# Performance work log

Measured on AMD Instinct MI355X. Metric: run time of the kernel, lower is better.

The kernel has to match this reference:

```python
import jax, jax.numpy as jnp
import numpy as np

N_HEAD = 16
T_THRESHOLD = 0.001


def setup_inputs() -> dict:
    key = jax.random.key(0)
    k_x, k_wa, k_ba, k_wp, k_bp = jax.random.split(key, 5)
    B, P, L, R = 8, 1024, 4, 256
    C = L * R  # n_embd = 1024
    s = 1.0 / np.sqrt(C)
    return {
        "x": jax.random.normal(k_x, (B, P, L, R), dtype=jnp.float32),
        "w_attn": jax.random.normal(k_wa, (C, 3 * C), dtype=jnp.float32) * s,
        "b_attn": jax.random.normal(k_ba, (3 * C,), dtype=jnp.float32) * 0.01,
        "w_proj": jax.random.normal(k_wp, (C, C), dtype=jnp.float32) * s,
        "b_proj": jax.random.normal(k_bp, (C,), dtype=jnp.float32) * 0.01,
    }


def reference(x, w_attn, b_attn, w_proj, b_proj):
    B, P, L, R = x.shape
    C = L * R
    H = N_HEAD
    hd = C // H
    xf = x.reshape(B, P, C)                      # (B, T, C)
    qkv = xf @ w_attn + b_attn                   # (B, T, 3C)
    q, k, v = jnp.split(qkv, 3, axis=-1)
    # (B, H, T, hd)
    q = q.reshape(B, P, H, hd).transpose(0, 2, 1, 3)
    k = k.reshape(B, P, H, hd).transpose(0, 2, 1, 3)
    v = v.reshape(B, P, H, hd).transpose(0, 2, 1, 3)
    att = jnp.einsum("bhqd,bhkd->bhqk", q, k) * (1.0 / np.sqrt(hd))
    att = jax.nn.softmax(att, axis=-1)
    att = jax.nn.relu(att - T_THRESHOLD)         # post-softmax thresholding
    y = jnp.einsum("bhqk,bhkd->bhqd", att, v)    # (B, H, T, hd)
    y = y.transpose(0, 2, 1, 3).reshape(B, P, C)
    y = y @ w_proj + b_proj
    return y.reshape(B, P, L, R)
```

## Files before the change

kernel.cpp:

```cpp
#include <hip/hip_runtime.h>


typedef _Float16 half8 __attribute__((ext_vector_type(8)));
typedef _Float16 half4_t __attribute__((ext_vector_type(4)));
typedef float floatx4 __attribute__((ext_vector_type(4)));
typedef float floatx16 __attribute__((ext_vector_type(16)));
typedef unsigned int uint4v __attribute__((ext_vector_type(4)));

__device__ __forceinline__ void gl2lds16(const void* gsrc, void* lds) {
    __builtin_amdgcn_global_load_lds(
        (const __attribute__((address_space(1))) unsigned int*)gsrc,
        (__attribute__((address_space(3))) unsigned int*)lds,
        16, 0, 0);
}

__device__ __forceinline__ unsigned pkh(float a, float b) {
    _Float16 ha = (_Float16)a, hb = (_Float16)b;
    unsigned short ua = __builtin_bit_cast(unsigned short, ha);
    unsigned short ub = __builtin_bit_cast(unsigned short, hb);
    return (unsigned)ua | ((unsigned)ub << 16);
}

__global__ __launch_bounds__(256) void prep(const float4* __restrict__ x4,
                                            _Float16* __restrict__ xh,
                                            const float* __restrict__ wa,
                                            _Float16* __restrict__ waT,
                                            const float* __restrict__ wp,
                                            _Float16* __restrict__ wpT) {
    __shared__ _Float16 t[64 * 65];
    int bid = blockIdx.x;
    if (bid < 4096) {
        int idx = bid * 256 + threadIdx.x;
#pragma unroll
        for (int i = idx; i < 2097152; i += 1048576) {
            float4 v = x4[i];
            half4_t h = { (_Float16)v.x, (_Float16)v.y, (_Float16)v.z, (_Float16)v.w };
            *(half4_t*)(xh + (size_t)i * 4) = h;
        }
    } else {
        int tt = bid - 4096;
        int by = tt & 15, bx = tt >> 4;
        const float* in = wa; _Float16* out = waT; int C = 3072;
        if (bx >= 48) { bx -= 48; in = wp; out = wpT; C = 1024; }
#pragma unroll
        for (int it = 0; it < 16; ++it) {
            int idx = it * 256 + threadIdx.x;
            int r = idx >> 6, c = idx & 63;
            t[c * 65 + r] = (_Float16)in[(size_t)(by * 64 + r) * C + bx * 64 + c];
        }
        __syncthreads();
#pragma unroll
        for (int it = 0; it < 16; ++it) {
            int idx = it * 256 + threadIdx.x;
            int rn = idx >> 6, ck = idx & 63;
            out[(size_t)(bx * 64 + rn) * 1024 + by * 64 + ck] = t[rn * 65 + ck];
        }
    }
}

#define GBAR __builtin_amdgcn_s_barrier()
#define WLGKM do { asm volatile("s_waitcnt lgkmcnt(0)" ::: "memory"); } while (0)
#define WVM2  do { asm volatile("s_waitcnt vmcnt(2)"   ::: "memory"); } while (0)
#define WVM4  do { asm volatile("s_waitcnt vmcnt(4)"   ::: "memory"); } while (0)
#define WVM0  do { asm volatile("s_waitcnt vmcnt(0)"   ::: "memory"); } while (0)


#define WLDA(buf, rg)                                                                         \
    do {                                                                                      \
        _Pragma("unroll") for (int i = 0; i < 4; ++i) {                                       \
            int r_ = wm * 128 + ((rg) * 4 + i) * 16 + l15;                                    \
            _Pragma("unroll") for (int kk = 0; kk < 2; ++kk)                                  \
                a[i][kk] = *(const half8*)(sA + (buf) * 32768 + r_ * 128 +                    \
                                           ((((kk << 2) + quad) ^ (r_ & 7)) << 4));           \
        }                                                                                     \
    } while (0)

#define WLDB(buf, cg, bb)                                                                     \
    do {                                                                                      \
        _Pragma("unroll") for (int j = 0; j < 2; ++j) {                                       \
            int r_ = wn * 64 + ((cg) * 2 + j) * 16 + l15;                                     \
            _Pragma("unroll") for (int kk = 0; kk < 2; ++kk)                                  \
                bb[j][kk] = *(const half8*)(sB + (buf) * 32768 + r_ * 128 +                   \
                                            ((((kk << 2) + quad) ^ (r_ & 7)) << 4));          \
        }                                                                                     \
    } while (0)

#define WMMA(rg, cg, bb)                                                                      \
    do {                                                                                      \
        __builtin_amdgcn_s_setprio(1);                                                        \
        _Pragma("unroll") for (int kk = 0; kk < 2; ++kk)                                      \
            _Pragma("unroll") for (int i = 0; i < 4; ++i)                                     \
                _Pragma("unroll") for (int j = 0; j < 2; ++j)                                  \
                    acc[(rg) * 4 + i][(cg) * 2 + j] = __builtin_amdgcn_mfma_f32_16x16x32_f16( \
                        a[i][kk], bb[j][kk], acc[(rg) * 4 + i][(cg) * 2 + j], 0, 0, 0);       \
        __builtin_amdgcn_s_setprio(0);                                                        \
    } while (0)

__global__ __launch_bounds__(512, 2) void gemm_qkv(const _Float16* __restrict__ A,
                                                   const _Float16* __restrict__ BT,
                                                   const float* __restrict__ bias,
                                                   _Float16* __restrict__ qno,
                                                   _Float16* __restrict__ kPo,
                                                   _Float16* __restrict__ vPo) {
    __shared__ __attribute__((aligned(16))) char lds[131072];
    char* sA = lds;
    char* sB = lds + 65536;
    int tid = threadIdx.x;
    int W = tid >> 6, lane = tid & 63, quad = lane >> 4, l15 = lane & 15;
    int wm = W >> 2, wn = W & 3;
    int flat = blockIdx.y * 12 + blockIdx.x;
    int swz = (flat & 7) * 48 + (flat >> 3);
    int m0 = (swz / 12) * 256, n0 = (swz % 12) * 256;

    auto stA = [&](int buf, int half, int k0) {
#pragma unroll
        for (int rnd = 0; rnd < 2; ++rnd) {
            int c = rnd * 512 + tid;
            int row = c >> 3;
            int q = (c & 7) ^ (row & 7);
            const _Float16* src = A + (size_t)(m0 + half * 128 + row) * 1024 + k0 + q * 8;
            int off = __builtin_amdgcn_readfirstlane(buf * 32768 + half * 16384 +
                                                     rnd * 8192 + (W << 10));
            gl2lds16(src, sA + off);
        }
    };
    auto stB = [&](int buf, int half, int k0) {
#pragma unroll
        for (int rnd = 0; rnd < 2; ++rnd) {
            int c = rnd * 512 + tid;
            int row = c >> 3;
            int q = (c & 7) ^ (row & 7);
            const _Float16* src = BT + (size_t)(n0 + half * 128 + row) * 1024 + k0 + q * 8;
            int off = __builtin_amdgcn_readfirstlane(buf * 32768 + half * 16384 +
                                                     rnd * 8192 + (W << 10));
            gl2lds16(src, sB + off);
        }
    };

    half8 a[4][2], b0[2][2], b1[2][2];
    floatx4 acc[8][4] = {};

    stA(0, 0, 0); stA(0, 1, 0);
    stB(0, 0, 0); stB(0, 1, 0);
    stB(1, 0, 64); stB(1, 1, 64);
    WVM4;
    GBAR;

#pragma unroll 1
    for (int t = 0; t < 16; t += 2) {
        int k1 = (t + 1) << 6;
        int k2 = ((t + 2) & 15) << 6;
        int k3 = ((t + 3) & 15) << 6;
        WLDA(0, 0); WLDB(0, 0, b0); stA(1, 0, k1);
        GBAR; WLGKM; WMMA(0, 0, b0); GBAR;
        WLDB(0, 1, b1); stA(1, 1, k1);
        GBAR; WLGKM; WMMA(0, 1, b1); GBAR;
        WLDA(0, 1); stB(0, 0, k2);
        GBAR; WLGKM; WMMA(1, 1, b1); GBAR;
        stB(0, 1, k2); WVM4;
        GBAR; WLGKM; WMMA(1, 0, b0); GBAR;
        WLDA(1, 0); WLDB(1, 0, b0); stA(0, 0, k2);
        GBAR; WLGKM; WMMA(0, 0, b0); GBAR;
        WLDB(1, 1, b1); stA(0, 1, k2);
        GBAR; WLGKM; WMMA(0, 1, b1); GBAR;
        WLDA(1, 1); stB(1, 0, k3);
        GBAR; WLGKM; WMMA(1, 1, b1); GBAR;
        stB(1, 1, k3); WVM4;
        GBAR; WLGKM; WMMA(1, 0, b0); GBAR;
    }

    WVM0;
    GBAR;
    int sec = n0 >> 10;
    int b = m0 >> 10;
    int tb = m0 & 1023;
#pragma unroll 1
    for (int p = 0; p < 2; ++p) {
        if (p) __syncthreads();
        if (sec == 2) {
            if ((wn >> 1) == p) {
#pragma unroll
                for (int cf = 0; cf < 4; ++cf) {
                    int lc = (wn & 1) * 64 + cf * 16 + l15;
                    float bv = bias[n0 + wn * 64 + cf * 16 + l15];
#pragma unroll
                    for (int rf = 0; rf < 8; ++rf) {
                        int m = wm * 128 + rf * 16 + quad * 4;
                        half4_t h4;
#pragma unroll
                        for (int r = 0; r < 4; ++r) h4[r] = (_Float16)(acc[rf][cf][r] + bv);
                        *(half4_t*)(lds + lc * 528 + m * 2) = h4;
                    }
                }
            }
            __syncthreads();
            int l15v = tid & 15;
            int moct = W * 4 + ((tid >> 4) & 3);
            int t = tb + moct * 8;
            int kbv = (t >> 5) & 31, quad_v = (t >> 3) & 3;
            int nbV = (n0 & 1023) + p * 128;
#pragma unroll
            for (int i = 0; i < 8; ++i) {
                int hh = i >> 2, cf = i & 3;
                int n = hh * 64 + cf * 16 + l15v;
                half8 v = *(const half8*)(lds + n * 528 + (moct << 4));
                int gcol = nbV + n;
                int h = gcol >> 6, d = gcol & 63;
                size_t chunk = (size_t)((b * 16 + h) * 32 + kbv) * 256 +
                               (d >> 4) * 64 + quad_v * 16 + (d & 15);
                *(half8*)(vPo + chunk * 8) = v;
            }
        } else {
            if ((wn >> 1) == p) {
#pragma unroll
                for (int cf = 0; cf < 4; ++cf) {
                    int lc = (wn & 1) * 64 + cf * 16 + l15;
                    float bv = bias[n0 + wn * 64 + cf * 16 + l15];
#pragma unroll
                    for (int rf = 0; rf < 8; ++rf) {
                        int m = wm * 128 + rf * 16 + quad * 4;
#pragma unroll
                        for (int r = 0; r < 4; ++r)
                            *(_Float16*)(lds + (m + r) * 272 + lc * 2) =
                                (_Float16)(acc[rf][cf][r] + bv);
                    }
                }
            }
            __syncthreads();
            int nb = (n0 & 1023) + p * 128;
            if (sec == 0) {
                int noct = tid & 15;
#pragma unroll
                for (int i = 0; i < 8; ++i) {
                    int m = i * 32 + (tid >> 4);
                    half8 v = *(const half8*)(lds + m * 272 + (noct << 4));
                    *(half8*)(qno + (size_t)(b * 1024 + tb + m) * 1024 + nb + noct * 8) = v;
                }
            } else {
                int l15k = tid & 15, noct = (tid >> 4) & 15;
#pragma unroll
                for (int i = 0; i < 8; ++i) {
                    int mb = i * 2 + (tid >> 8);
                    int m = mb * 16 + l15k;
                    half8 v = *(const half8*)(lds + m * 272 + (noct << 4));
                    int gcol = nb + noct * 8;
                    int h = gcol >> 6, d0 = gcol & 63;
                    int t = tb + m;
                    size_t chunk = (size_t)((b * 16 + h) * 64 + (t >> 4)) * 128 +
                                   (d0 >> 5) * 64 + ((d0 >> 3) & 3) * 16 + l15k;
                    *(half8*)(kPo + chunk * 8) = v;
                }
            }
        }
    }
}

#define LDA(buf, rg)                                                                          \
    do {                                                                                      \
        _Pragma("unroll") for (int i = 0; i < 2; ++i) {                                       \
            int r_ = wm * 64 + ((rg) * 2 + i) * 16 + l15;                                     \
            _Pragma("unroll") for (int kk = 0; kk < 2; ++kk)                                  \
                a[i][kk] = *(const half8*)(sA + (buf) * 32768 + r_ * 128 +                    \
                                           ((((kk << 2) + quad) ^ (r_ & 7)) << 4));           \
        }                                                                                     \
    } while (0)

#define LDB(buf, cg, bb)                                                                      \
    do {                                                                                      \
        _Pragma("unroll") for (int j = 0; j < 2; ++j) {                                       \
            int r_ = wn * 64 + ((cg) * 2 + j) * 16 + l15;                                     \
            _Pragma("unroll") for (int kk = 0; kk < 2; ++kk)                                  \
                bb[j][kk] = *(const half8*)(sB + (buf) * 16384 + r_ * 128 +                   \
                                            ((((kk << 2) + quad) ^ (r_ & 7)) << 4));          \
        }                                                                                     \
    } while (0)

#define MMA(rg, cg, bb)                                                                       \
    do {                                                                                      \
        __builtin_amdgcn_s_setprio(1);                                                        \
        _Pragma("unroll") for (int kk = 0; kk < 2; ++kk)                                      \
            _Pragma("unroll") for (int i = 0; i < 2; ++i)                                     \
                _Pragma("unroll") for (int j = 0; j < 2; ++j)                                  \
                    acc[(rg) * 2 + i][(cg) * 2 + j] = __builtin_amdgcn_mfma_f32_16x16x32_f16( \
                        a[i][kk], bb[j][kk], acc[(rg) * 2 + i][(cg) * 2 + j], 0, 0, 0);       \
        __builtin_amdgcn_s_setprio(0);                                                        \
    } while (0)

__global__ __launch_bounds__(512, 2) void gemm_proj(const _Float16* __restrict__ A,
                                                    const _Float16* __restrict__ BT,
                                                    const float* __restrict__ bias,
                                                    float* __restrict__ o0, int N) {
    __shared__ __attribute__((aligned(16))) char lds[98304];
    char* sA = lds;
    char* sB = lds + 65536;
    int tid = threadIdx.x;
    int W = tid >> 6, lane = tid & 63, quad = lane >> 4, l15 = lane & 15;
    int wm = W >> 1, wn = W & 1;
    int flat = blockIdx.y * 8 + blockIdx.x;
    int swz = (flat & 7) * 32 + (flat >> 3);
    int m0 = (swz >> 3) * 256, n0 = (swz & 7) * 128;

    auto stA = [&](int buf, int half, int k0) {
#pragma unroll
        for (int rnd = 0; rnd < 2; ++rnd) {
            int c = rnd * 512 + tid;
            int row = c >> 3;
            int q = (c & 7) ^ (row & 7);
            const _Float16* src = A + (size_t)(m0 + half * 128 + row) * 1024 + k0 + q * 8;
            int off = __builtin_amdgcn_readfirstlane(buf * 32768 + half * 16384 +
                                                     rnd * 8192 + (W << 10));
            gl2lds16(src, sA + off);
        }
    };
    auto stB = [&](int buf, int half, int k0) {
        int row = tid >> 3;
        int q = (tid & 7) ^ (row & 7);
        const _Float16* src = BT + (size_t)(n0 + half * 64 + row) * 1024 + k0 + q * 8;
        int off = __builtin_amdgcn_readfirstlane(buf * 16384 + half * 8192 + (W << 10));
        gl2lds16(src, sB + off);
    };

    half8 a[2][2], b0[2][2], b1[2][2];
    floatx4 acc[4][4] = {};

    stA(0, 0, 0); stA(0, 1, 0);
    stB(0, 0, 0); stB(0, 1, 0);
    stB(1, 0, 64); stB(1, 1, 64);
    WVM2;
    GBAR;

#pragma unroll 1
    for (int t = 0; t < 16; t += 2) {
        int k1 = (t + 1) << 6;
        int k2 = ((t + 2) & 15) << 6;
        int k3 = ((t + 3) & 15) << 6;
        LDA(0, 0); LDB(0, 0, b0); stA(1, 0, k1);
        GBAR; WLGKM; MMA(0, 0, b0); GBAR;
        LDB(0, 1, b1); stA(1, 1, k1);
        GBAR; WLGKM; MMA(0, 1, b1); GBAR;
        LDA(0, 1); stB(0, 0, k2);
        GBAR; WLGKM; MMA(1, 1, b1); GBAR;
        stB(0, 1, k2); WVM2;
        GBAR; WLGKM; MMA(1, 0, b0); GBAR;
        LDA(1, 0); LDB(1, 0, b0); stA(0, 0, k2);
        GBAR; WLGKM; MMA(0, 0, b0); GBAR;
        LDB(1, 1, b1); stA(0, 1, k2);
        GBAR; WLGKM; MMA(0, 1, b1); GBAR;
        LDA(1, 1); stB(1, 0, k3);
        GBAR; WLGKM; MMA(1, 1, b1); GBAR;
        stB(1, 1, k3); WVM2;
        GBAR; WLGKM; MMA(1, 0, b0); GBAR;
    }

#pragma unroll
    for (int cf = 0; cf < 4; ++cf) {
        int gn = n0 + wn * 64 + cf * 16 + l15;
        float bv = bias[gn];
#pragma unroll
        for (int rf = 0; rf < 4; ++rf) {
            int gmBase = m0 + wm * 64 + rf * 16 + quad * 4;
#pragma unroll
            for (int r = 0; r < 4; ++r)
                o0[(size_t)(gmBase + r) * N + gn] = acc[rf][cf][r] + bv;
        }
    }
}

__global__ __launch_bounds__(512, 4) void attn(const _Float16* __restrict__ qn,
                                               const _Float16* __restrict__ kP,
                                               const _Float16* __restrict__ vP,
                                               _Float16* __restrict__ y) {
    __shared__ __attribute__((aligned(16))) char red[65536];
    __shared__ float lsum[8][32];
    int tid = threadIdx.x;
    int W = tid >> 6, lane = tid & 63;
    int l31 = lane & 31, hi = lane >> 5;
    int flat = blockIdx.y * 32 + blockIdx.x;
    int swz = (flat & 7) * 512 + (flat >> 3);
    int qt = swz & 31, bh = swz >> 5;
    int b = bh >> 4, h = bh & 15;
    int q0 = qt * 32;

    const _Float16* kPb = kP + (size_t)bh * 8192 * 8;
    const _Float16* vPb = vP + (size_t)bh * 8192 * 8;

    half8 bq[4];
#pragma unroll
    for (int ks = 0; ks < 4; ++ks)
        bq[ks] = *(const half8*)(qn + (size_t)(b * 1024 + q0 + l31) * 1024 +
                                 h * 64 + ks * 16 + hi * 8);

    half8 pd[4][2];
    float lpA = 0.f, lpB = 0.f;
#pragma unroll
    for (int kb = 0; kb < 4; ++kb) {
        int cbase = (W * 8 + kb * 2 + (l31 >> 4)) * 128 + (l31 & 15);
        half8 ak0 = *(const half8*)(kPb + (size_t)(cbase + hi * 16) * 8);
        half8 ak1 = *(const half8*)(kPb + (size_t)(cbase + (2 + hi) * 16) * 8);
        half8 ak2 = *(const half8*)(kPb + (size_t)(cbase + 64 + hi * 16) * 8);
        half8 ak3 = *(const half8*)(kPb + (size_t)(cbase + 64 + (2 + hi) * 16) * 8);
        floatx16 s = {};
        __builtin_amdgcn_s_setprio(1);
        s = __builtin_amdgcn_mfma_f32_32x32x16_f16(ak0, bq[0], s, 0, 0, 0);
        s = __builtin_amdgcn_mfma_f32_32x32x16_f16(ak1, bq[1], s, 0, 0, 0);
        s = __builtin_amdgcn_mfma_f32_32x32x16_f16(ak2, bq[2], s, 0, 0, 0);
        s = __builtin_amdgcn_mfma_f32_32x32x16_f16(ak3, bq[3], s, 0, 0, 0);
        __builtin_amdgcn_s_setprio(0);
        float e[16];
#pragma unroll
        for (int r = 0; r < 16; ++r)
            e[r] = __builtin_amdgcn_exp2f(s[r] * 0.18033688f);
        lpA += ((e[0] + e[1]) + (e[2] + e[3])) + ((e[4] + e[5]) + (e[6] + e[7]));
        lpB += ((e[8] + e[9]) + (e[10] + e[11])) + ((e[12] + e[13]) + (e[14] + e[15]));
#pragma unroll
        for (int c2 = 0; c2 < 2; ++c2) {
            int o = c2 * 8;
            unsigned P01 = pkh(e[o + 0], e[o + 1]);
            unsigned P23 = pkh(e[o + 2], e[o + 3]);
            unsigned P45 = pkh(e[o + 4], e[o + 5]);
            unsigned P67 = pkh(e[o + 6], e[o + 7]);
            asm("v_permlane32_swap_b32 %0, %1" : "+v"(P01), "+v"(P45));
            asm("v_permlane32_swap_b32 %0, %1" : "+v"(P23), "+v"(P67));
            uint4v F = { P01, P23, P45, P67 };
            pd[kb][c2] = __builtin_bit_cast(half8, F);
        }
    }
    {
        float lp = lpA + lpB;
        lp += __shfl_xor(lp, 32);
        if (lane < 32) lsum[W][l31] = lp;
    }
    __syncthreads();

    half8 inv8, t8, z8;
#pragma unroll
    for (int j = 0; j < 8; ++j) { t8[j] = (_Float16)(-0.001f); z8[j] = (_Float16)0.f; }
    {
        float l = 0.f;
#pragma unroll
        for (int w = 0; w < 8; ++w) l += lsum[w][l31];
        _Float16 invh = (_Float16)(1.0f / l);
#pragma unroll
        for (int j = 0; j < 8; ++j) inv8[j] = invh;
    }
#pragma unroll
    for (int kb = 0; kb < 4; ++kb)
#pragma unroll
        for (int c2 = 0; c2 < 2; ++c2) {
            pd[kb][c2] = pd[kb][c2] * inv8 + t8;
            pd[kb][c2] = __builtin_elementwise_max(pd[kb][c2], z8);
        }

    floatx16 acc0 = {}, acc1 = {};
#pragma unroll
    for (int kb = 0; kb < 4; ++kb)
#pragma unroll
        for (int c2 = 0; c2 < 2; ++c2) {
            int kc = (W * 4 + kb) * 2 + c2;
            int vbase = (kc >> 1) * 256 + (l31 >> 4) * 64 + ((kc & 1) * 2 + hi) * 16 +
                        (l31 & 15);
            half8 bv0 = *(const half8*)(vPb + (size_t)vbase * 8);
            half8 bv1 = *(const half8*)(vPb + (size_t)(vbase + 128) * 8);
            __builtin_amdgcn_s_setprio(1);
            acc0 = __builtin_amdgcn_mfma_f32_32x32x16_f16(pd[kb][c2], bv0, acc0, 0, 0, 0);
            acc1 = __builtin_amdgcn_mfma_f32_32x32x16_f16(pd[kb][c2], bv1, acc1, 0, 0, 0);
            __builtin_amdgcn_s_setprio(0);
        }

#pragma unroll
    for (int r = 0; r < 16; ++r) {
        int q = (r & 3) + 8 * (r >> 2) + 4 * hi;
        *(float*)(red + q * 2048 + W * 256 + l31 * 4) = acc0[r];
        *(float*)(red + q * 2048 + W * 256 + 128 + l31 * 4) = acc1[r];
    }
    __syncthreads();
    {
        int e4 = tid * 4;
        int r = e4 >> 6, c = e4 & 63;
        floatx4 s = {};
#pragma unroll
        for (int w = 0; w < 8; ++w)
            s += *(const floatx4*)(red + r * 2048 + w * 256 + c * 4);
        half4_t hv = { (_Float16)s[0], (_Float16)s[1], (_Float16)s[2], (_Float16)s[3] };
        *(half4_t*)(y + (size_t)(b * 1024 + q0 + r) * 1024 + h * 64 + c) = hv;
    }
}

extern "C" void kernel_launch(void* const* d_in, const int* in_sizes, int n_in,
                              void* d_out, int out_size, void* d_ws, size_t ws_size,
                              hipStream_t stream) {
    const float* x  = (const float*)d_in[0];
    const float* wa = (const float*)d_in[1];
    const float* ba = (const float*)d_in[2];
    const float* wp = (const float*)d_in[3];
    const float* bp = (const float*)d_in[4];
    float* out = (float*)d_out;

    char* ws = (char*)d_ws;
    _Float16* y   = (_Float16*)(ws);
    _Float16* qn  = (_Float16*)(ws + 16777216);
    _Float16* kP  = (_Float16*)(ws + 33554432);
    _Float16* vP  = (_Float16*)(ws + 50331648);
    _Float16* waT = (_Float16*)(ws + 67108864);
    _Float16* wpT = (_Float16*)(ws + 73400320);
    _Float16* xh  = (_Float16*)(ws + 75497472);

    prep<<<5120, 256, 0, stream>>>((const float4*)x, xh, wa, waT, wp, wpT);
    gemm_qkv<<<dim3(12, 32), 512, 0, stream>>>(xh, waT, ba, qn, kP, vP);
    attn<<<dim3(32, 128), 512, 0, stream>>>(qn, kP, vP, y);
    gemm_proj<<<dim3(8, 32), 512, 0, stream>>>(y, wpT, bp, out, 1024);
}
```

Before: 262.6 us.

## Give each wave its own query tile and iterate all keys with two-pass softmax

Measured after the change: 257.9 us. No clear change (-1.8%).

```diff
diff --git a/kernel.cpp b/kernel.cpp
--- a/kernel.cpp
+++ b/kernel.cpp
@@ -370,14 +370,13 @@
                                                const _Float16* __restrict__ kP,
                                                const _Float16* __restrict__ vP,
                                                _Float16* __restrict__ y) {
-    __shared__ __attribute__((aligned(16))) char red[65536];
-    __shared__ float lsum[8][32];
     int tid = threadIdx.x;
     int W = tid >> 6, lane = tid & 63;
     int l31 = lane & 31, hi = lane >> 5;
-    int flat = blockIdx.y * 32 + blockIdx.x;
-    int swz = (flat & 7) * 512 + (flat >> 3);
-    int qt = swz & 31, bh = swz >> 5;
+    int flat = blockIdx.x;
+    int swz = (flat & 7) * 64 + (flat >> 3);
+    int bh = swz >> 2;
+    int qt = (swz & 3) * 8 + W;
     int b = bh >> 4, h = bh & 15;
     int q0 = qt * 32;
 
@@ -390,11 +389,10 @@
         bq[ks] = *(const half8*)(qn + (size_t)(b * 1024 + q0 + l31) * 1024 +
                                  h * 64 + ks * 16 + hi * 8);
 
-    half8 pd[4][2];
     float lpA = 0.f, lpB = 0.f;
-#pragma unroll
-    for (int kb = 0; kb < 4; ++kb) {
-        int cbase = (W * 8 + kb * 2 + (l31 >> 4)) * 128 + (l31 & 15);
+#pragma unroll 2
+    for (int kb = 0; kb < 32; ++kb) {
+        int cbase = (kb * 2 + (l31 >> 4)) * 128 + (l31 & 15);
         half8 ak0 = *(const half8*)(kPb + (size_t)(cbase + hi * 16) * 8);
         half8 ak1 = *(const half8*)(kPb + (size_t)(cbase + (2 + hi) * 16) * 8);
         half8 ak2 = *(const half8*)(kPb + (size_t)(cbase + 64 + hi * 16) * 8);
@@ -412,6 +410,38 @@
             e[r] = __builtin_amdgcn_exp2f(s[r] * 0.18033688f);
         lpA += ((e[0] + e[1]) + (e[2] + e[3])) + ((e[4] + e[5]) + (e[6] + e[7]));
         lpB += ((e[8] + e[9]) + (e[10] + e[11])) + ((e[12] + e[13]) + (e[14] + e[15]));
+    }
+    half8 inv8, t8, z8;
+#pragma unroll
+    for (int j = 0; j < 8; ++j) { t8[j] = (_Float16)(-0.001f); z8[j] = (_Float16)0.f; }
+    {
+        float lp = lpA + lpB;
+        lp += __shfl_xor(lp, 32);
+        _Float16 invh = (_Float16)(1.0f / lp);
+#pragma unroll
+        for (int j = 0; j < 8; ++j) inv8[j] = invh;
+    }
+
+    floatx16 acc0 = {}, acc1 = {};
+#pragma unroll 2
+    for (int kb = 0; kb < 32; ++kb) {
+        int cbase = (kb * 2 + (l31 >> 4)) * 128 + (l31 & 15);
+        half8 ak0 = *(const half8*)(kPb + (size_t)(cbase + hi * 16) * 8);
+        half8 ak1 = *(const half8*)(kPb + (size_t)(cbase + (2 + hi) * 16) * 8);
+        half8 ak2 = *(const half8*)(kPb + (size_t)(cbase + 64 + hi * 16) * 8);
+        half8 ak3 = *(const half8*)(kPb + (size_t)(cbase + 64 + (2 + hi) * 16) * 8);
+        floatx16 s = {};
+        __builtin_amdgcn_s_setprio(1);
+        s = __builtin_amdgcn_mfma_f32_32x32x16_f16(ak0, bq[0], s, 0, 0, 0);
+        s = __builtin_amdgcn_mfma_f32_32x32x16_f16(ak1, bq[1], s, 0, 0, 0);
+        s = __builtin_amdgcn_mfma_f32_32x32x16_f16(ak2, bq[2], s, 0, 0, 0);
+        s = __builtin_amdgcn_mfma_f32_32x32x16_f16(ak3, bq[3], s, 0, 0, 0);
+        __builtin_amdgcn_s_setprio(0);
+        float e[16];
+#pragma unroll
+        for (int r = 0; r < 16; ++r)
+            e[r] = __builtin_amdgcn_exp2f(s[r] * 0.18033688f);
+        half8 pd[2];
 #pragma unroll
         for (int c2 = 0; c2 < 2; ++c2) {
             int o = c2 * 8;
@@ -422,67 +452,28 @@
             asm("v_permlane32_swap_b32 %0, %1" : "+v"(P01), "+v"(P45));
             asm("v_permlane32_swap_b32 %0, %1" : "+v"(P23), "+v"(P67));
             uint4v F = { P01, P23, P45, P67 };
-            pd[kb][c2] = __builtin_bit_cast(half8, F);
-        }
-    }
-    {
-        float lp = lpA + lpB;
-        lp += __shfl_xor(lp, 32);
-        if (lane < 32) lsum[W][l31] = lp;
-    }
-    __syncthreads();
-
-    half8 inv8, t8, z8;
-#pragma unroll
-    for (int j = 0; j < 8; ++j) { t8[j] = (_Float16)(-0.001f); z8[j] = (_Float16)0.f; }
-    {
-        float l = 0.f;
-#pragma unroll
-        for (int w = 0; w < 8; ++w) l += lsum[w][l31];
-        _Float16 invh = (_Float16)(1.0f / l);
-#pragma unroll
-        for (int j = 0; j < 8; ++j) inv8[j] = invh;
-    }
-#pragma unroll
-    for (int kb = 0; kb < 4; ++kb)
+            pd[c2] = __builtin_bit_cast(half8, F);
+            pd[c2] = pd[c2] * inv8 + t8;
+            pd[c2] = __builtin_elementwise_max(pd[c2], z8);
+        }
 #pragma unroll
         for (int c2 = 0; c2 < 2; ++c2) {
-            pd[kb][c2] = pd[kb][c2] * inv8 + t8;
-            pd[kb][c2] = __builtin_elementwise_max(pd[kb][c2], z8);
-        }
-
-    floatx16 acc0 = {}, acc1 = {};
-#pragma unroll
-    for (int kb = 0; kb < 4; ++kb)
-#pragma unroll
-        for (int c2 = 0; c2 < 2; ++c2) {
-            int kc = (W * 4 + kb) * 2 + c2;
-            int vbase = (kc >> 1) * 256 + (l31 >> 4) * 64 + ((kc & 1) * 2 + hi) * 16 +
-                        (l31 & 15);
+            int vbase = kb * 256 + (l31 >> 4) * 64 + (c2 * 2 + hi) * 16 + (l31 & 15);
             half8 bv0 = *(const half8*)(vPb + (size_t)vbase * 8);
             half8 bv1 = *(const half8*)(vPb + (size_t)(vbase + 128) * 8);
             __builtin_amdgcn_s_setprio(1);
-            acc0 = __builtin_amdgcn_mfma_f32_32x32x16_f16(pd[kb][c2], bv0, acc0, 0, 0, 0);
-            acc1 = __builtin_amdgcn_mfma_f32_32x32x16_f16(pd[kb][c2], bv1, acc1, 0, 0, 0);
+            acc0 = __builtin_amdgcn_mfma_f32_32x32x16_f16(pd[c2], bv0, acc0, 0, 0, 0);
+            acc1 = __builtin_amdgcn_mfma_f32_32x32x16_f16(pd[c2], bv1, acc1, 0, 0, 0);
             __builtin_amdgcn_s_setprio(0);
         }
-
+    }
+
+    _Float16* yb = y + (size_t)(b * 1024 + q0) * 1024 + h * 64;
 #pragma unroll
     for (int r = 0; r < 16; ++r) {
         int q = (r & 3) + 8 * (r >> 2) + 4 * hi;
-        *(float*)(red + q * 2048 + W * 256 + l31 * 4) = acc0[r];
-        *(float*)(red + q * 2048 + W * 256 + 128 + l31 * 4) = acc1[r];
-    }
-    __syncthreads();
-    {
-        int e4 = tid * 4;
-        int r = e4 >> 6, c = e4 & 63;
-        floatx4 s = {};
-#pragma unroll
-        for (int w = 0; w < 8; ++w)
-            s += *(const floatx4*)(red + r * 2048 + w * 256 + c * 4);
-        half4_t hv = { (_Float16)s[0], (_Float16)s[1], (_Float16)s[2], (_Float16)s[3] };
-        *(half4_t*)(y + (size_t)(b * 1024 + q0 + r) * 1024 + h * 64 + c) = hv;
+        yb[(size_t)q * 1024 + l31] = (_Float16)acc0[r];
+        yb[(size_t)q * 1024 + 32 + l31] = (_Float16)acc1[r];
     }
 }
 
@@ -507,6 +498,6 @@
 
     prep<<<5120, 256, 0, stream>>>((const float4*)x, xh, wa, waT, wp, wpT);
     gemm_qkv<<<dim3(12, 32), 512, 0, stream>>>(xh, waT, ba, qn, kP, vP);
-    attn<<<dim3(32, 128), 512, 0, stream>>>(qn, kP, vP, y);
+    attn<<<512, 512, 0, stream>>>(qn, kP, vP, y);
     gemm_proj<<<dim3(8, 32), 512, 0, stream>>>(y, wpT, bp, out, 1024);
 }
```
